# Optimization experiments

Measured on AMD Instinct MI355X. Metric: run time of the kernel, lower is better.

## Reference

```python
import jax, jax.numpy as jnp
import numpy as np

B, S, D = 8, 2048, 128
NEG = -1e9

def setup_inputs() -> dict:
    key = jax.random.key(0)
    kq, kk, kv = jax.random.split(key, 3)
    query = jax.random.normal(kq, (B, S, D), dtype=jnp.float32)
    k_ = jax.random.normal(kk, (B, S, D), dtype=jnp.float32)
    value = jax.random.normal(kv, (B, S, D), dtype=jnp.float32)
    mask = jnp.tril(jnp.ones((S, S), dtype=jnp.int32))  # causal (seq_len, seq_len)
    return {"query": query, "key": k_, "value": value, "mask": mask}

def reference(query, key, value, mask):
    d_k = query.shape[-1]
    # scores: [B, S, S]
    scores = jnp.einsum('bqd,bkd->bqk', query, key) / jnp.sqrt(jnp.asarray(d_k, jnp.float32))
    scores = jnp.where(mask == 0, jnp.asarray(NEG, scores.dtype), scores)
    p_attn = jax.nn.softmax(scores, axis=-1)
    # dropout p=0.0 -> identity
    return jnp.einsum('bqk,bkd->bqd', p_attn, value)
```

## Files before the change

### kernel.cpp

```cpp
#include <hip/hip_runtime.h>


#define BATCH 8
#define SEQ   2048
#define DIM   128
#define CK    256

typedef _Float16 v4h __attribute__((ext_vector_type(4)));
typedef _Float16 v8h __attribute__((ext_vector_type(8)));
typedef float    v4f __attribute__((ext_vector_type(4)));

#define QF_H 0u
#define KF_H 2097152u
#define VF_H 4194304u
#define OP_H 6291456u
#define ML_B 31457280u
#define WS_NEED 31752192u

__constant__ const float kScale = 0.08838834764831845f;

__global__ __launch_bounds__(256) void prepass(
    const float* __restrict__ K, const float* __restrict__ V,
    _Float16* __restrict__ wsh)
{
    const int b = blockIdx.x;
    const int t = threadIdx.x;
    if (b < 1024) {
        __shared__ float tile[16][132];
        const int batch = b >> 7, vt = b & 127;
        const float* src = V + ((size_t)batch * SEQ + vt * 16) * DIM;
        const int row = t >> 4, col = (t & 15) * 8;
        *(v4f*)&tile[row][col]     = *(const v4f*)(src + (size_t)row * DIM + col);
        *(v4f*)&tile[row][col + 4] = *(const v4f*)(src + (size_t)row * DIM + col + 4);
        __syncthreads();
        const int n = t >> 4, p = (t >> 2) & 3, qd = t & 3;
        v8h h;
        #pragma unroll
        for (int j = 0; j < 8; ++j) {
            const int d  = 32 * p + 16 * (j >> 2) + n;
            const int kk = qd * 4 + (j & 3);
            h[j] = (_Float16)tile[kk][d];
        }
        const int w = n * 64 + ((p * 16 + qd * 4) ^ ((n & 7) << 2));
        *(v8h*)(wsh + VF_H + (size_t)batch * 262144 + vt * 2048 + w * 2) = h;
    } else {
        const int i = (b - 1024) * 256 + t;
        const int seg = i & 15, row = i >> 4;
        const float* src = K + (size_t)row * DIM + seg * 8;
        v4f a = *(const v4f*)src;
        v4f c = *(const v4f*)(src + 4);
        v8h h;
        #pragma unroll
        for (int j = 0; j < 4; ++j) {
            h[j]     = (_Float16)a[j];
            h[j + 4] = (_Float16)c[j];
        }
        const int w = (seg * 4) ^ ((row & 7) << 2);
        *(v8h*)(wsh + KF_H + (size_t)row * DIM + w * 2) = h;
    }
}

__device__ __forceinline__ void dma16(const _Float16* g, const _Float16* l) {
    __builtin_amdgcn_global_load_lds(
        (const __attribute__((address_space(1))) unsigned int*)g,
        (__attribute__((address_space(3))) unsigned int*)(unsigned int)(uintptr_t)l,
        16, 0, 0);
}

__global__ __launch_bounds__(512, 4) void attn_chunk(
    const float* __restrict__ Q, const _Float16* __restrict__ wsh,
    float* __restrict__ Ml, _Float16* __restrict__ Op)
{
    __shared__ __align__(16) _Float16 lds[16384];

    const int batch = blockIdx.x & 7;
    int g = blockIdx.x >> 3;
    int c = 0;
    for (; c < 8; ++c) { const int cnt = 16 - 2 * c; if (g < cnt) break; g -= cnt; }
    const int wave = threadIdx.x >> 6;
    const int qt = 16 * c + g * 8 + wave;
    const int q0 = qt * 16;
    const int kbeg = c * CK;

    const int lane = threadIdx.x & 63;
    const int n = lane & 15, quad = lane >> 4;
    const size_t bo = (size_t)batch * SEQ * DIM;

    const _Float16* Kf = wsh + KF_H + bo;
    const _Float16* Vf = wsh + VF_H + bo;

    v8h qa[4];
    {
        const float* qp = Q + bo + (size_t)(q0 + n) * DIM + quad * 8;
        #pragma unroll
        for (int p = 0; p < 4; ++p) {
            v4f a = *(const v4f*)(qp + p * 32);
            v4f b2 = *(const v4f*)(qp + p * 32 + 4);
            v8h h;
            #pragma unroll
            for (int j = 0; j < 4; ++j) {
                h[j]     = (_Float16)(a[j] * kScale);
                h[j + 4] = (_Float16)(b2[j] * kScale);
            }
            qa[p] = h;
        }
    }

    const int isv = wave >> 2, idx = wave & 3;
    const _Float16* gseg = (isv ? (Vf + (size_t)(kbeg >> 4) * 2048)
                                : (Kf + (size_t)kbeg * DIM)) + idx * 1024;
    const int ldsseg = isv * 4096 + idx * 1024;

    int koff[4];
    #pragma unroll
    for (int p = 0; p < 4; ++p)
        koff[p] = n * 128 + (((quad * 4 + p * 16) ^ ((n & 7) << 2)) << 1);

    float l_run = 0.0f;
    v4f of[8];
    #pragma unroll
    for (int dc = 0; dc < 8; ++dc) of[dc] = (v4f){0.f, 0.f, 0.f, 0.f};

    const int qn0 = q0 + n - kbeg;
    const int kq = quad * 4;

    #pragma unroll
    for (int i = 0; i < 2; ++i)
        dma16(gseg + i * 512 + lane * 8, &lds[ldsseg + i * 512]);

    #pragma unroll
    for (int kb = 0; kb < 8; ++kb) {
        __syncthreads();
        if (kb < 7) {
            const _Float16* gs = gseg + (kb + 1) * 4096;
            const int lb = ((kb + 1) & 1) * 8192 + ldsseg;
            #pragma unroll
            for (int i = 0; i < 2; ++i)
                dma16(gs + i * 512 + lane * 8, &lds[lb + i * 512]);
        }
        const int base = (kb & 1) * 8192;
        #pragma unroll
        for (int t16 = 0; t16 < 2; ++t16) {
            v4f s = (v4f){0.f, 0.f, 0.f, 0.f};
            __builtin_amdgcn_s_setprio(1);
            #pragma unroll
            for (int p = 0; p < 4; ++p) {
                v8h kf = *(const v8h*)&lds[base + t16 * 2048 + koff[p]];
                s = __builtin_amdgcn_mfma_f32_16x16x32_f16(kf, qa[p], s, 0, 0, 0);
            }
            __builtin_amdgcn_s_setprio(0);
            v4h pf;
            float ps = 0.f;
            #pragma unroll
            for (int r = 0; r < 4; ++r) {
                const float sv = (kb * 32 + t16 * 16 + kq + r > qn0) ? -1e30f : s[r];
                const float p = __expf(sv);
                ps += p;
                pf[r] = (_Float16)p;
            }
            l_run += ps;
            __builtin_amdgcn_s_setprio(1);
            #pragma unroll
            for (int p = 0; p < 4; ++p) {
                v8h vv = *(const v8h*)&lds[base + 4096 + t16 * 2048 + koff[p]];
                v4h vlo = __builtin_shufflevector(vv, vv, 0, 1, 2, 3);
                v4h vhi = __builtin_shufflevector(vv, vv, 4, 5, 6, 7);
                of[2 * p]     = __builtin_amdgcn_mfma_f32_16x16x16f16(vlo, pf, of[2 * p], 0, 0, 0);
                of[2 * p + 1] = __builtin_amdgcn_mfma_f32_16x16x16f16(vhi, pf, of[2 * p + 1], 0, 0, 0);
            }
            __builtin_amdgcn_s_setprio(0);
        }
    }

    l_run += __shfl_xor(l_run, 16);
    l_run += __shfl_xor(l_run, 32);

    const int rs = (2048 * c - 128 * c * (c - 1)) * 8
                 + batch * (2048 - CK * c) + (q0 + n - CK * c);
    _Float16* op = Op + (size_t)rs * DIM;
    #pragma unroll
    for (int dc = 0; dc < 8; ++dc) {
        v4h o;
        #pragma unroll
        for (int r = 0; r < 4; ++r) o[r] = (_Float16)of[dc][r];
        *(v4h*)(op + dc * 16 + quad * 4) = o;
    }
    if (quad == 0) Ml[rs] = l_run;
}

__global__ __launch_bounds__(256) void combine(
    const _Float16* __restrict__ Op, const float* __restrict__ Ml,
    float* __restrict__ O)
{
    const int gid = blockIdx.x * 256 + threadIdx.x;
    const size_t e = (size_t)gid * 8;
    const int d = (int)(e & 127);
    const int q = (int)((e >> 7) & 2047);
    const int b = (int)(e >> 18);
    const int nc = (q >> 8) + 1;
    float L = 0.f;
    float acc[8] = {0.f, 0.f, 0.f, 0.f, 0.f, 0.f, 0.f, 0.f};
    for (int c = 0; c < nc; ++c) {
        const int rs = (2048 * c - 128 * c * (c - 1)) * 8 + b * (2048 - 256 * c) + (q - 256 * c);
        L += Ml[rs];
        v8h o = *(const v8h*)(Op + (size_t)rs * DIM + d);
        #pragma unroll
        for (int r = 0; r < 8; ++r) acc[r] += (float)o[r];
    }
    const float rl = 1.0f / L;
    v4f o0, o1;
    #pragma unroll
    for (int r = 0; r < 4; ++r) { o0[r] = acc[r] * rl; o1[r] = acc[r + 4] * rl; }
    *(v4f*)(O + e)     = o0;
    *(v4f*)(O + e + 4) = o1;
}

__global__ __launch_bounds__(128) void attn_fwd(
    const float* __restrict__ Q, const float* __restrict__ K,
    const float* __restrict__ V, float* __restrict__ O)
{
    const int batch = blockIdx.x & 7;
    const int qb    = blockIdx.x >> 3;
    const int tid   = threadIdx.x;
    const int wave  = tid >> 6;
    const int lane  = tid & 63;
    const int n     = lane & 15;
    const int quad  = lane >> 4;

    const int q0      = qb * 32 + wave * 16;
    const int my_last = qb * 2 + wave;
    const int nt      = qb * 2 + 2;

    const size_t bo = (size_t)batch * SEQ * DIM;

    __shared__ __align__(16) _Float16 Ks[16 * 136];
    __shared__ __align__(16) _Float16 Vt[128 * 20];
    typedef _Float16 v2h __attribute__((ext_vector_type(2)));

    v4h qf[8];
    {
        const float* qp = Q + bo + (size_t)(q0 + n) * DIM + quad * 4;
        #pragma unroll
        for (int dc = 0; dc < 8; ++dc) {
            v4f qv = *(const v4f*)(qp + dc * 16);
            v4h h;
            #pragma unroll
            for (int i = 0; i < 4; ++i) h[i] = (_Float16)(qv[i] * kScale);
            qf[dc] = h;
        }
    }

    float m_run = -1e30f, l_run = 0.0f;
    v4f of[8];
    #pragma unroll
    for (int dc = 0; dc < 8; ++dc) of[dc] = (v4f){0.f, 0.f, 0.f, 0.f};

    const int krow = tid >> 3;
    const int kcol = (tid & 7) * 16;
    const int vr   = (tid >> 4) * 2;
    const int vc   = (tid & 15) * 4;

    for (int tk = 0; tk < nt; ++tk) {
        const int k0 = tk * 16;
        {
            const float* kp = K + bo + (size_t)(k0 + krow) * DIM + kcol;
            v4f k0v = *(const v4f*)(kp);
            v4f k1v = *(const v4f*)(kp + 4);
            v4f k2v = *(const v4f*)(kp + 8);
            v4f k3v = *(const v4f*)(kp + 12);
            const float* vp = V + bo + (size_t)(k0 + vr) * DIM + vc;
            v4f va0 = *(const v4f*)(vp);
            v4f va1 = *(const v4f*)(vp + DIM);
            v4f vb0 = *(const v4f*)(vp + 64);
            v4f vb1 = *(const v4f*)(vp + DIM + 64);

            v8h h0, h1;
            #pragma unroll
            for (int i = 0; i < 4; ++i) {
                h0[i]     = (_Float16)k0v[i];
                h0[i + 4] = (_Float16)k1v[i];
                h1[i]     = (_Float16)k2v[i];
                h1[i + 4] = (_Float16)k3v[i];
            }
            *(v8h*)&Ks[krow * 136 + kcol]     = h0;
            *(v8h*)&Ks[krow * 136 + kcol + 8] = h1;

            #pragma unroll
            for (int i = 0; i < 4; ++i) {
                v2h p0 = { (_Float16)va0[i], (_Float16)va1[i] };
                v2h p1 = { (_Float16)vb0[i], (_Float16)vb1[i] };
                *(v2h*)&Vt[(vc + i) * 20 + vr]      = p0;
                *(v2h*)&Vt[(vc + 64 + i) * 20 + vr] = p1;
            }
        }
        __syncthreads();

        if (tk <= my_last) {
            v4f s = (v4f){0.f, 0.f, 0.f, 0.f};
            #pragma unroll
            for (int dc = 0; dc < 8; ++dc) {
                v4h kf = *(const v4h*)&Ks[n * 136 + dc * 16 + quad * 4];
                s = __builtin_amdgcn_mfma_f32_16x16x16f16(kf, qf[dc], s, 0, 0, 0);
            }
            if (tk == my_last) {
                #pragma unroll
                for (int r = 0; r < 4; ++r)
                    if (quad * 4 + r > n) s[r] = -1e30f;
            }
            float tm = fmaxf(fmaxf(s[0], s[1]), fmaxf(s[2], s[3]));
            tm = fmaxf(tm, __shfl_xor(tm, 16));
            tm = fmaxf(tm, __shfl_xor(tm, 32));
            const float m_new = fmaxf(m_run, tm);
            const float alpha = __expf(m_run - m_new);
            v4f p;
            #pragma unroll
            for (int r = 0; r < 4; ++r) p[r] = __expf(s[r] - m_new);
            float ps = p[0] + p[1] + p[2] + p[3];
            ps += __shfl_xor(ps, 16);
            ps += __shfl_xor(ps, 32);
            l_run = l_run * alpha + ps;
            m_run = m_new;

            v4h pf;
            #pragma unroll
            for (int r = 0; r < 4; ++r) pf[r] = (_Float16)p[r];

            #pragma unroll
            for (int dc = 0; dc < 8; ++dc) {
                v4h vf = *(const v4h*)&Vt[(dc * 16 + n) * 20 + quad * 4];
                of[dc] *= alpha;
                of[dc] = __builtin_amdgcn_mfma_f32_16x16x16f16(vf, pf, of[dc], 0, 0, 0);
            }
        }
        __syncthreads();
    }

    const float rl = 1.0f / l_run;
    float* op = O + bo + (size_t)(q0 + n) * DIM + quad * 4;
    #pragma unroll
    for (int dc = 0; dc < 8; ++dc) {
        v4f o = of[dc] * rl;
        *(v4f*)(op + dc * 16) = o;
    }
}

extern "C" void kernel_launch(void* const* d_in, const int* in_sizes, int n_in,
                              void* d_out, int out_size, void* d_ws, size_t ws_size,
                              hipStream_t stream) {
    const float* Q = (const float*)d_in[0];
    const float* K = (const float*)d_in[1];
    const float* V = (const float*)d_in[2];
    float* Out = (float*)d_out;

    if (ws_size >= (size_t)WS_NEED) {
        _Float16* wsh = (_Float16*)d_ws;
        _Float16* Op  = wsh + OP_H;
        float*    Ml  = (float*)((char*)d_ws + ML_B);
        prepass<<<dim3(2048), dim3(256), 0, stream>>>(K, V, wsh);
        attn_chunk<<<dim3(8 * 72), dim3(512), 0, stream>>>(Q, wsh, Ml, Op);
        combine<<<dim3(1024), dim3(256), 0, stream>>>(Op, Ml, Out);
    } else {
        attn_fwd<<<dim3(BATCH * (SEQ / 32)), dim3(128), 0, stream>>>(Q, K, V, Out);
    }
}
```

Measured before the change: 113.2 us.

## Fuse split-K combine into attention kernel via atomic last-block reduction

Removes the separate combine kernel. Each attention-chunk block that owns the only chunk for its query group writes normalized fp32 output directly. Other blocks store their fp16 partials, then increment an atomic counter, and the last arriving block reduces all chunk partials for that 128-row group. Counters are zeroed in the prepass. This saves a kernel launch and the extra pass over the partials, at the cost of a threadfence, atomics, and a serialized tail reduction inside the last block.

Measured after the change: 287.9 us. +154.3%, slower.

```diff
diff --git a/kernel.cpp b/kernel.cpp
--- a/kernel.cpp
+++ b/kernel.cpp
@@ -15,7 +15,8 @@
 #define VF_H 4194304u
 #define OP_H 6291456u
 #define ML_B 31457280u
-#define WS_NEED 31752192u
+#define CNT_B 31752192u
+#define WS_NEED 31752704u
 
 __constant__ const float kScale = 0.08838834764831845f;
 
@@ -44,6 +45,8 @@
         const int w = n * 64 + ((p * 16 + qd * 4) ^ ((n & 7) << 2));
         *(v8h*)(wsh + VF_H + (size_t)batch * 262144 + vt * 2048 + w * 2) = h;
     } else {
+        if (b == 1024 && t < 128)
+            ((unsigned*)((char*)wsh + CNT_B))[t] = 0u;
         const int i = (b - 1024) * 256 + t;
         const int seg = i & 15, row = i >> 4;
         const float* src = K + (size_t)row * DIM + seg * 8;
@@ -69,9 +72,11 @@
 
 __global__ __launch_bounds__(512, 4) void attn_chunk(
     const float* __restrict__ Q, const _Float16* __restrict__ wsh,
-    float* __restrict__ Ml, _Float16* __restrict__ Op)
+    float* __restrict__ Ml, _Float16* __restrict__ Op,
+    float* __restrict__ Out, unsigned* __restrict__ Cnt)
 {
     __shared__ __align__(16) _Float16 lds[16384];
+    __shared__ unsigned winflag;
 
     const int batch = blockIdx.x & 7;
     int g = blockIdx.x >> 3;
@@ -175,6 +180,18 @@
     l_run += __shfl_xor(l_run, 16);
     l_run += __shfl_xor(l_run, 32);
 
+    const int G = 2 * c + g;
+    const int need = (G >> 1) + 1;
+
+    if (need == 1) {
+        const float rl = 1.0f / l_run;
+        float* op = Out + bo + (size_t)(q0 + n) * DIM + quad * 4;
+        #pragma unroll
+        for (int dc = 0; dc < 8; ++dc)
+            *(v4f*)(op + dc * 16) = of[dc] * rl;
+        return;
+    }
+
     const int rs = (2048 * c - 128 * c * (c - 1)) * 8
                  + batch * (2048 - CK * c) + (q0 + n - CK * c);
     _Float16* op = Op + (size_t)rs * DIM;
@@ -186,33 +203,45 @@
         *(v4h*)(op + dc * 16 + quad * 4) = o;
     }
     if (quad == 0) Ml[rs] = l_run;
-}
-
-__global__ __launch_bounds__(256) void combine(
-    const _Float16* __restrict__ Op, const float* __restrict__ Ml,
-    float* __restrict__ O)
-{
-    const int gid = blockIdx.x * 256 + threadIdx.x;
-    const size_t e = (size_t)gid * 8;
-    const int d = (int)(e & 127);
-    const int q = (int)((e >> 7) & 2047);
-    const int b = (int)(e >> 18);
-    const int nc = (q >> 8) + 1;
+
+    __threadfence();
+    __syncthreads();
+    if (threadIdx.x == 0) {
+        const unsigned old = atomicAdd(&Cnt[(batch << 4) + G], 1u);
+        winflag = (old == (unsigned)(need - 1)) ? 1u : 0u;
+    }
+    __syncthreads();
+    if (winflag == 0) return;
+
+    __threadfence();
+    const int tid = threadIdx.x;
+    const int q  = (G << 7) + (tid >> 2);
+    const int d0 = (tid & 3) << 5;
     float L = 0.f;
-    float acc[8] = {0.f, 0.f, 0.f, 0.f, 0.f, 0.f, 0.f, 0.f};
-    for (int c = 0; c < nc; ++c) {
-        const int rs = (2048 * c - 128 * c * (c - 1)) * 8 + b * (2048 - 256 * c) + (q - 256 * c);
-        L += Ml[rs];
-        v8h o = *(const v8h*)(Op + (size_t)rs * DIM + d);
-        #pragma unroll
-        for (int r = 0; r < 8; ++r) acc[r] += (float)o[r];
+    float acc[32];
+    #pragma unroll
+    for (int j = 0; j < 32; ++j) acc[j] = 0.f;
+    for (int cc = 0; cc < need; ++cc) {
+        const int rsc = (2048 * cc - 128 * cc * (cc - 1)) * 8
+                      + batch * (2048 - CK * cc) + (q - CK * cc);
+        L += Ml[rsc];
+        const _Float16* pp = Op + (size_t)rsc * DIM + d0;
+        #pragma unroll
+        for (int v = 0; v < 4; ++v) {
+            v8h o = *(const v8h*)(pp + v * 8);
+            #pragma unroll
+            for (int r = 0; r < 8; ++r) acc[v * 8 + r] += (float)o[r];
+        }
     }
     const float rl = 1.0f / L;
-    v4f o0, o1;
-    #pragma unroll
-    for (int r = 0; r < 4; ++r) { o0[r] = acc[r] * rl; o1[r] = acc[r + 4] * rl; }
-    *(v4f*)(O + e)     = o0;
-    *(v4f*)(O + e + 4) = o1;
+    float* oo = Out + bo + (size_t)q * DIM + d0;
+    #pragma unroll
+    for (int v = 0; v < 8; ++v) {
+        v4f w;
+        #pragma unroll
+        for (int r = 0; r < 4; ++r) w[r] = acc[v * 4 + r] * rl;
+        *(v4f*)(oo + v * 4) = w;
+    }
 }
 
 __global__ __launch_bounds__(128) void attn_fwd(
@@ -356,9 +385,9 @@
         _Float16* wsh = (_Float16*)d_ws;
         _Float16* Op  = wsh + OP_H;
         float*    Ml  = (float*)((char*)d_ws + ML_B);
+        unsigned* Cnt = (unsigned*)((char*)d_ws + CNT_B);
         prepass<<<dim3(2048), dim3(256), 0, stream>>>(K, V, wsh);
-        attn_chunk<<<dim3(8 * 72), dim3(512), 0, stream>>>(Q, wsh, Ml, Op);
-        combine<<<dim3(1024), dim3(256), 0, stream>>>(Op, Ml, Out);
+        attn_chunk<<<dim3(8 * 72), dim3(512), 0, stream>>>(Q, wsh, Ml, Op, Out, Cnt);
     } else {
         attn_fwd<<<dim3(BATCH * (SEQ / 32)), dim3(128), 0, stream>>>(Q, K, V, Out);
     }
```
